# Kernel tuning notes

Hardware: AMD Instinct MI355X
Metric: run time of the kernel (lower is better)

The kernel has to match this reference:

```python
import jax, jax.numpy as jnp
import numpy as np

N_PROJ, DET_H, DET_W = 360, 512, 512
VOL = (128, 128, 128)  # (Z, Y, X)
SID, SDD = 750.0, 1200.0  # source-isocenter / source-detector distance (mm)


def _make_trajectory():
    # Circular cone-beam orbit: P = K [R | -R s], 3x4 per projection.
    cu, cv = (DET_W - 1) / 2.0, (DET_H - 1) / 2.0
    K = np.array([[SDD, 0.0, cu], [0.0, SDD, cv], [0.0, 0.0, 1.0]])
    mats = []
    for th in np.linspace(0.0, 2.0 * np.pi, N_PROJ, endpoint=False):
        c, s = np.cos(th), np.sin(th)
        src = SID * np.array([c, s, 0.0])
        # camera rows: u-axis, v-axis, optical axis (source -> isocenter)
        R = np.array([[-s, c, 0.0], [0.0, 0.0, 1.0], [-c, -s, 0.0]])
        P = K @ np.hstack([R, (-R @ src)[:, None]])
        mats.append(P)
    return np.stack(mats).astype(np.float32)


def setup_inputs() -> dict:
    key = jax.random.key(0)
    sino = jax.random.normal(key, (1, N_PROJ, DET_H, DET_W), dtype=jnp.float32)
    spacing = np.array([2.0, 2.0, 2.0], np.float32)  # (z, y, x) mm
    origin = (-(np.array(VOL, np.float32) - 1.0) / 2.0 * spacing)  # centered volume
    return {
        "input": sino,
        "volume_shape": np.array(VOL, np.int64),
        "volume_origin": jnp.asarray(origin),
        "volume_spacing": jnp.asarray(spacing),
        "trajectory": jnp.asarray(_make_trajectory()),
        "projection_multiplier": jnp.float32(np.pi / N_PROJ),
        "step_size": jnp.float32(1.0),
    }


def _bilinear(img, u, v):
    # img: [B,H,W]; u,v: [Z,Y,X] continuous detector coords. Zero outside detector.
    H, W = img.shape[-2], img.shape[-1]
    u0 = jnp.floor(u); v0 = jnp.floor(v)
    fu = u - u0; fv = v - v0
    u0i = u0.astype(jnp.int32); v0i = v0.astype(jnp.int32)
    valid = (u >= 0) & (u <= W - 1) & (v >= 0) & (v <= H - 1)
    u0c = jnp.clip(u0i, 0, W - 1); u1c = jnp.clip(u0i + 1, 0, W - 1)
    v0c = jnp.clip(v0i, 0, H - 1); v1c = jnp.clip(v0i + 1, 0, H - 1)
    g = lambda vi, ui: img[:, vi, ui]  # gather -> [B,Z,Y,X]
    top = g(v0c, u0c) * (1.0 - fu) + g(v0c, u1c) * fu
    bot = g(v1c, u0c) * (1.0 - fu) + g(v1c, u1c) * fu
    return jnp.where(valid, top * (1.0 - fv) + bot * fv, 0.0)


def reference(input, volume_shape, volume_origin, volume_spacing, trajectory,
              projection_multiplier, step_size):
    Z, Y, X = int(volume_shape[0]), int(volume_shape[1]), int(volume_shape[2])
    oz, oy, ox = volume_origin[0], volume_origin[1], volume_origin[2]
    sz, sy, sx = volume_spacing[0], volume_spacing[1], volume_spacing[2]
    # world coordinates of voxel centers, broadcastable to [Z,Y,X]
    wz = (oz + sz * jnp.arange(Z, dtype=jnp.float32))[:, None, None]
    wy = (oy + sy * jnp.arange(Y, dtype=jnp.float32))[None, :, None]
    wx = (ox + sx * jnp.arange(X, dtype=jnp.float32))[None, None, :]
    B = input.shape[0]

    def step(acc, xs):
        P, sino_n = xs  # P: [3,4], sino_n: [B,H,W]
        un = P[0, 0] * wx + P[0, 1] * wy + P[0, 2] * wz + P[0, 3]
        vn = P[1, 0] * wx + P[1, 1] * wy + P[1, 2] * wz + P[1, 3]
        t  = P[2, 0] * wx + P[2, 1] * wy + P[2, 2] * wz + P[2, 3]  # ray depth
        u = un / t
        v = vn / t
        # FDK-style distance weighting: projection_multiplier / depth^2
        val = _bilinear(sino_n, u, v) * (projection_multiplier / (t * t))
        return acc + val, None

    acc0 = jnp.zeros((B, Z, Y, X), jnp.float32)
    sino_per_proj = jnp.swapaxes(input, 0, 1)  # [N_proj, B, H, W]
    out, _ = jax.lax.scan(step, acc0, (trajectory, sino_per_proj))
    return out
```

## Files before the change

kernel.cpp:

```cpp
#include <hip/hip_runtime.h>

#define NPROJ 360
#define DH 512
#define DW 512
#define VZ 128
#define VY 128
#define VX 128
#define ZC 8

typedef float f2_u __attribute__((ext_vector_type(2), aligned(4)));

__global__ __launch_bounds__(256, 4)
void cone_bp_kernel(const float* __restrict__ sino,
                    const float* __restrict__ origin,
                    const float* __restrict__ spacing,
                    const float* __restrict__ traj,
                    const float* __restrict__ pm_p,
                    float* __restrict__ out)
{
    const int bid  = blockIdx.x;
    const int slab = bid & 7;
    const int rem  = bid >> 3;
    const int zis  = rem & 1;
    const int xy   = rem >> 1;
    const int bx   = xy & 7;
    const int by   = xy >> 3;

    const int t    = threadIdx.x;
    const int w    = t >> 6;
    const int l    = t & 63;
    const int x    = bx * 16 + ((w & 1) << 3) + (l & 7);
    const int y    = by * 16 + ((w >> 1) << 3) + (l >> 3);
    const int z0   = slab * 16 + zis * ZC;

    const float oz = origin[0], oy = origin[1], ox = origin[2];
    const float sz = spacing[0], sy = spacing[1], sx = spacing[2];
    const float pm = pm_p[0];

    const float wx  = ox + sx * (float)x;
    const float wy  = oy + sy * (float)y;
    const float wz0 = oz + sz * (float)z0;

    float acc[ZC];
#pragma unroll
    for (int j = 0; j < ZC; ++j) acc[j] = 0.0f;

    const float* P = traj;
    const float* img = sino;
    for (int n = 0; n < NPROJ; ++n, P += 12, img += DH * DW) {
        const float p00 = P[0], p01 = P[1], p02 = P[2],  p03 = P[3];
        const float p10 = P[4], p11 = P[5], p12 = P[6],  p13 = P[7];
        const float p20 = P[8], p21 = P[9], p22 = P[10], p23 = P[11];

        float un = p00 * wx + p01 * wy + p02 * wz0 + p03;
        float vn = p10 * wx + p11 * wy + p12 * wz0 + p13;
        float tt = p20 * wx + p21 * wy + p22 * wz0 + p23;

        if (p02 == 0.0f && p22 == 0.0f) {
            const float rt = 1.0f / tt;
            const float u  = un * rt;
            const float wgt = pm * rt * rt;
            const bool uval = (u >= 0.0f) && (u <= (float)(DW - 1));
            const float u0f = floorf(u);
            const float fu  = u - u0f;
            const int   u0  = (int)u0f;
            const int u0c = min(max(u0, 0), DW - 1);
            const int u1c = min(max(u0 + 1, 0), DW - 1);
            const int uc  = min(max(u0, 0), DW - 2);
            const bool s0 = (u0c == uc);
            const bool s1 = (u1c == uc);
            const float dvn = p12 * sz;

            f2_u  pr0[ZC], pr1[ZC];
            float fv[ZC];
            bool  valid[ZC];
#pragma unroll
            for (int j = 0; j < ZC; ++j) {
                const float v = fmaf((float)j, dvn, vn) * rt;
                const float v0f = floorf(v);
                fv[j] = v - v0f;
                const int v0 = (int)v0f;
                valid[j] = uval && (v >= 0.0f) && (v <= (float)(DH - 1));
                const int v0c = min(max(v0, 0), DH - 1);
                const int v1c = min(max(v0 + 1, 0), DH - 1);
                pr0[j] = *(const f2_u*)(img + v0c * DW + uc);
                pr1[j] = *(const f2_u*)(img + v1c * DW + uc);
            }
#pragma unroll
            for (int j = 0; j < ZC; ++j) {
                const float t00 = s0 ? pr0[j].x : pr0[j].y;
                const float t01 = s1 ? pr0[j].x : pr0[j].y;
                const float t10 = s0 ? pr1[j].x : pr1[j].y;
                const float t11 = s1 ? pr1[j].x : pr1[j].y;
                const float top = t00 + fu * (t01 - t00);
                const float bot = t10 + fu * (t11 - t10);
                const float s   = top + fv[j] * (bot - top);
                acc[j] += valid[j] ? (s * wgt) : 0.0f;
            }
        } else {
            const float dun = p02 * sz, dvn = p12 * sz, dtt = p22 * sz;
#pragma unroll
            for (int j = 0; j < ZC; ++j) {
                const float jf = (float)j;
                const float unj = fmaf(jf, dun, un);
                const float vnj = fmaf(jf, dvn, vn);
                const float ttj = fmaf(jf, dtt, tt);
                const float rt = 1.0f / ttj;
                const float u = unj * rt;
                const float v = vnj * rt;
                const float wgt = pm * rt * rt;
                const bool valid = (u >= 0.0f) && (u <= (float)(DW - 1)) &&
                                   (v >= 0.0f) && (v <= (float)(DH - 1));
                const float u0f = floorf(u), v0f = floorf(v);
                const float fu = u - u0f, fv = v - v0f;
                const int u0 = (int)u0f, v0 = (int)v0f;
                const int u0c = min(max(u0, 0), DW - 1);
                const int u1c = min(max(u0 + 1, 0), DW - 1);
                const int v0c = min(max(v0, 0), DH - 1);
                const int v1c = min(max(v0 + 1, 0), DH - 1);
                const float* r0 = img + v0c * DW;
                const float* r1 = img + v1c * DW;
                const float t00 = r0[u0c], t01 = r0[u1c];
                const float t10 = r1[u0c], t11 = r1[u1c];
                const float top = t00 + fu * (t01 - t00);
                const float bot = t10 + fu * (t11 - t10);
                const float s   = top + fv * (bot - top);
                acc[j] += valid ? (s * wgt) : 0.0f;
            }
        }
    }

#pragma unroll
    for (int j = 0; j < ZC; ++j) {
        out[((size_t)(z0 + j) * VY + y) * VX + x] = acc[j];
    }
}

extern "C" void kernel_launch(void* const* d_in, const int* in_sizes, int n_in,
                              void* d_out, int out_size, void* d_ws, size_t ws_size,
                              hipStream_t stream) {
    const float* sino    = (const float*)d_in[0];
    const float* origin  = (const float*)d_in[2];
    const float* spacing = (const float*)d_in[3];
    const float* traj    = (const float*)d_in[4];
    const float* pm      = (const float*)d_in[5];
    float* out = (float*)d_out;

    dim3 block(256, 1, 1);
    dim3 grid(1024, 1, 1);
    cone_bp_kernel<<<grid, block, 0, stream>>>(sino, origin, spacing, traj, pm, out);
}
```

Measured before the change: 1.491 ms.

## Stage per-projection detector footprint into LDS and skip out-of-view projections

```diff
diff --git a/kernel.cpp b/kernel.cpp
--- a/kernel.cpp
+++ b/kernel.cpp
@@ -7,8 +7,13 @@
 #define VY 128
 #define VX 128
 #define ZC 8
+#define LROWS 60
+#define LPITCH 132
+#define LCOLS 128
 
 typedef float f2_u __attribute__((ext_vector_type(2), aligned(4)));
+typedef float f4_u __attribute__((ext_vector_type(4), aligned(4)));
+typedef float f4_a __attribute__((ext_vector_type(4), aligned(16)));
 
 __global__ __launch_bounds__(256, 4)
 void cone_bp_kernel(const float* __restrict__ sino,
@@ -18,6 +23,9 @@
                     const float* __restrict__ pm_p,
                     float* __restrict__ out)
 {
+    __shared__ __align__(16) float win[LROWS * LPITCH];
+    __shared__ unsigned meta[NPROJ];
+
     const int bid  = blockIdx.x;
     const int slab = bid & 7;
     const int rem  = bid >> 3;
@@ -41,6 +49,56 @@
     const float wy  = oy + sy * (float)y;
     const float wz0 = oz + sz * (float)z0;
 
+    const float bwx0 = ox + sx * (float)(bx * 16);
+    const float bwx1 = ox + sx * (float)(bx * 16 + 15);
+    const float bwy0 = oy + sy * (float)(by * 16);
+    const float bwy1 = oy + sy * (float)(by * 16 + 15);
+
+    for (int p = t; p < NPROJ; p += 256) {
+        const float* Pp = traj + 12 * p;
+        const float p00 = Pp[0], p01 = Pp[1], p02 = Pp[2],  p03 = Pp[3];
+        const float p10 = Pp[4], p11 = Pp[5], p12 = Pp[6],  p13 = Pp[7];
+        const float p20 = Pp[8], p21 = Pp[9], p22 = Pp[10], p23 = Pp[11];
+        unsigned m;
+        if (p02 == 0.0f && p22 == 0.0f) {
+            const float dvn = p12 * sz;
+            float umin = 1e30f, umax = -1e30f, vmin = 1e30f, vmax = -1e30f;
+            float tmin = 1e30f;
+#pragma unroll
+            for (int ci = 0; ci < 4; ++ci) {
+                const float cx = (ci & 1) ? bwx1 : bwx0;
+                const float cy = (ci & 2) ? bwy1 : bwy0;
+                const float un = p00 * cx + p01 * cy + p02 * wz0 + p03;
+                const float vn = p10 * cx + p11 * cy + p12 * wz0 + p13;
+                const float tt = p20 * cx + p21 * cy + p22 * wz0 + p23;
+                const float rt = 1.0f / tt;
+                const float uu  = un * rt;
+                const float va  = vn * rt;
+                const float vb  = fmaf((float)(ZC - 1), dvn, vn) * rt;
+                tmin = fminf(tmin, tt);
+                umin = fminf(umin, uu); umax = fmaxf(umax, uu);
+                vmin = fminf(vmin, fminf(va, vb));
+                vmax = fmaxf(vmax, fmaxf(va, vb));
+            }
+            const bool skip = (umax < -0.5f) || (umin > (float)(DW - 1) + 0.5f) ||
+                              (vmax < -0.5f) || (vmin > (float)(DH - 1) + 0.5f);
+            const int r_lo = min(max((int)floorf(vmin) - 1, 0), DH - 1);
+            const int r_hi = min(max((int)floorf(vmax) + 2, 0), DH - 1);
+            const int rows = r_hi - r_lo + 1;
+            const int c_lo = min(max((int)floorf(umin) - 1, 0), DW - 2);
+            const int c_hi = min(max((int)floorf(umax) + 2, 0), DW - 1);
+            const int cols = c_hi - c_lo + 1;
+            const bool fb = (tmin <= 0.0f) || (rows > LROWS) || (cols > LCOLS);
+            m = (unsigned)r_lo | ((unsigned)c_lo << 9) |
+                ((unsigned)min(rows, 127) << 18) |
+                (skip ? (1u << 25) : 0u) | (fb ? (1u << 26) : 0u);
+        } else {
+            m = (1u << 26);
+        }
+        meta[p] = m;
+    }
+    __syncthreads();
+
     float acc[ZC];
 #pragma unroll
     for (int j = 0; j < ZC; ++j) acc[j] = 0.0f;
@@ -48,6 +106,36 @@
     const float* P = traj;
     const float* img = sino;
     for (int n = 0; n < NPROJ; ++n, P += 12, img += DH * DW) {
+        const unsigned m = meta[n];
+        const bool skip = (m >> 25) & 1u;
+        const bool fb   = (m >> 26) & 1u;
+        const int r_lo  = m & 511;
+        const int c_lo  = (m >> 9) & 511;
+        const int rows  = (m >> 18) & 127;
+
+        __syncthreads();
+        if (!skip && !fb) {
+            if (n != NPROJ - 1) {
+                const int nch = rows << 5;
+                for (int c = t; c < nch; c += 256) {
+                    const int r  = c >> 5;
+                    const int c4 = (c & 31) << 2;
+                    const f4_u vq = *(const f4_u*)(img + (r_lo + r) * DW + (c_lo + c4));
+                    *(f4_a*)(&win[r * LPITCH + c4]) = vq;
+                }
+            } else {
+                const int nel = rows << 7;
+                for (int c = t; c < nel; c += 256) {
+                    const int r  = c >> 7;
+                    const int cc = c & 127;
+                    const int gc = min(c_lo + cc, DW - 1);
+                    win[r * LPITCH + cc] = img[(r_lo + r) * DW + gc];
+                }
+            }
+        }
+        __syncthreads();
+        if (skip) continue;
+
         const float p00 = P[0], p01 = P[1], p02 = P[2],  p03 = P[3];
         const float p10 = P[4], p11 = P[5], p12 = P[6],  p13 = P[7];
         const float p20 = P[8], p21 = P[9], p22 = P[10], p23 = P[11];
@@ -56,7 +144,7 @@
         float vn = p10 * wx + p11 * wy + p12 * wz0 + p13;
         float tt = p20 * wx + p21 * wy + p22 * wz0 + p23;
 
-        if (p02 == 0.0f && p22 == 0.0f) {
+        if (!fb) {
             const float rt = 1.0f / tt;
             const float u  = un * rt;
             const float wgt = pm * rt * rt;
@@ -70,6 +158,49 @@
             const bool s0 = (u0c == uc);
             const bool s1 = (u1c == uc);
             const float dvn = p12 * sz;
+            const int cbase = (uc - c_lo) - r_lo * LPITCH;
+
+            float t00[ZC], t01[ZC], t10[ZC], t11[ZC], fv[ZC];
+            bool  valid[ZC];
+#pragma unroll
+            for (int j = 0; j < ZC; ++j) {
+                const float v = fmaf((float)j, dvn, vn) * rt;
+                const float v0f = floorf(v);
+                fv[j] = v - v0f;
+                const int v0 = (int)v0f;
+                valid[j] = uval && (v >= 0.0f) && (v <= (float)(DH - 1));
+                const int v0c = min(max(v0, 0), DH - 1);
+                const int v1c = min(v0c + 1, DH - 1);
+                const int a0 = v0c * LPITCH + cbase;
+                const int a1 = v1c * LPITCH + cbase;
+                t00[j] = win[a0]; t01[j] = win[a0 + 1];
+                t10[j] = win[a1]; t11[j] = win[a1 + 1];
+            }
+#pragma unroll
+            for (int j = 0; j < ZC; ++j) {
+                const float q00 = s0 ? t00[j] : t01[j];
+                const float q01 = s1 ? t00[j] : t01[j];
+                const float q10 = s0 ? t10[j] : t11[j];
+                const float q11 = s1 ? t10[j] : t11[j];
+                const float top = q00 + fu * (q01 - q00);
+                const float bot = q10 + fu * (q11 - q10);
+                const float s   = top + fv[j] * (bot - top);
+                acc[j] += valid[j] ? (s * wgt) : 0.0f;
+            }
+        } else if (p02 == 0.0f && p22 == 0.0f) {
+            const float rt = 1.0f / tt;
+            const float u  = un * rt;
+            const float wgt = pm * rt * rt;
+            const bool uval = (u >= 0.0f) && (u <= (float)(DW - 1));
+            const float u0f = floorf(u);
+            const float fu  = u - u0f;
+            const int   u0  = (int)u0f;
+            const int u0c = min(max(u0, 0), DW - 1);
+            const int u1c = min(max(u0 + 1, 0), DW - 1);
+            const int uc  = min(max(u0, 0), DW - 2);
+            const bool s0 = (u0c == uc);
+            const bool s1 = (u1c == uc);
+            const float dvn = p12 * sz;
 
             f2_u  pr0[ZC], pr1[ZC];
             float fv[ZC];
@@ -88,12 +219,12 @@
             }
 #pragma unroll
             for (int j = 0; j < ZC; ++j) {
-                const float t00 = s0 ? pr0[j].x : pr0[j].y;
-                const float t01 = s1 ? pr0[j].x : pr0[j].y;
-                const float t10 = s0 ? pr1[j].x : pr1[j].y;
-                const float t11 = s1 ? pr1[j].x : pr1[j].y;
-                const float top = t00 + fu * (t01 - t00);
-                const float bot = t10 + fu * (t11 - t10);
+                const float q00 = s0 ? pr0[j].x : pr0[j].y;
+                const float q01 = s1 ? pr0[j].x : pr0[j].y;
+                const float q10 = s0 ? pr1[j].x : pr1[j].y;
+                const float q11 = s1 ? pr1[j].x : pr1[j].y;
+                const float top = q00 + fu * (q01 - q00);
+                const float bot = q10 + fu * (q11 - q10);
                 const float s   = top + fv[j] * (bot - top);
                 acc[j] += valid[j] ? (s * wgt) : 0.0f;
             }
```

New measurement: 1.468 ms. No clear change (-1.5%).
